# Kernel tuning notes

Measured on AMD Instinct MI355X. Metric: run time of the kernel, lower is better.

## Reference

```python
import jax, jax.numpy as jnp
import numpy as np

N_ENT = 50000
N_REL = 500
DIM = 128
B = 1024
N_EDGES = 800000
BN_EPS = 1e-5


def setup_inputs() -> dict:
    key = jax.random.key(0)
    ks = jax.random.split(key, 12)
    return {
        "E_emb": jax.random.normal(ks[0], (N_ENT, DIM), jnp.float32),
        "R_emb": jax.random.normal(ks[1], (N_REL, DIM), jnp.float32),
        "W1": jax.random.normal(ks[2], (DIM, DIM), jnp.float32) / np.sqrt(DIM),
        "b1": jax.random.normal(ks[3], (DIM,), jnp.float32) * 0.01,
        "W2": jax.random.normal(ks[4], (DIM, DIM), jnp.float32) / np.sqrt(DIM),
        "b2": jax.random.normal(ks[5], (DIM,), jnp.float32) * 0.01,
        "W": jax.random.normal(ks[6], (DIM, DIM), jnp.float32) / np.sqrt(DIM),
        "adj_vals": jax.random.uniform(ks[7], (N_EDGES,), jnp.float32) / 16.0,
        "bn0_gamma": jnp.ones((DIM,), jnp.float32),
        "bn0_beta": jnp.zeros((DIM,), jnp.float32),
        "bn1_gamma": jnp.ones((DIM,), jnp.float32),
        "bn1_beta": jnp.zeros((DIM,), jnp.float32),
        "batch_head": jax.random.randint(ks[8], (B,), 0, N_ENT, jnp.int32),
        "batch_rel": jax.random.randint(ks[9], (B,), 0, N_REL, jnp.int32),
        "init_ind": jnp.arange(N_ENT, dtype=jnp.int32),
        "adj_rows": jax.random.randint(ks[10], (N_EDGES,), 0, N_ENT, jnp.int32),
        "adj_cols": jax.random.randint(ks[11], (N_EDGES,), 0, N_ENT, jnp.int32),
    }


def _bn_eval(x, gamma, beta):
    # BatchNorm1d in eval mode with running_mean=0, running_var=1
    return x * (gamma / jnp.sqrt(1.0 + BN_EPS)) + beta


def _spmm(rows, cols, vals, dense):
    # out[i] = sum_{e: rows[e]==i} vals[e] * dense[cols[e]]
    gathered = dense[cols] * vals[:, None]  # [E, DIM]
    return jax.ops.segment_sum(gathered, rows, num_segments=N_ENT)


def reference(E_emb, R_emb, W1, b1, W2, b2, W, adj_vals,
              bn0_gamma, bn0_beta, bn1_gamma, bn1_beta,
              batch_head, batch_rel, init_ind, adj_rows, adj_cols):
    init_emb = E_emb[init_ind]                                  # [N, D]
    h = jax.nn.relu(_spmm(adj_rows, adj_cols, adj_vals, init_emb @ W1) + b1)
    h = jax.nn.relu(_spmm(adj_rows, adj_cols, adj_vals, h @ W2) + b2)
    final_emb = init_emb + h                                    # shortcut connection
    x = _bn_eval(final_emb[batch_head], bn0_gamma, bn0_beta)    # [B, D]
    r = R_emb[batch_rel]                                        # [B, D]
    W_mat = r @ W                                               # mat_vec_mul: [B, D]
    vm = _bn_eval(x * W_mat, bn1_gamma, bn1_beta)               # [B, D]
    dot = vm @ final_emb.T                                      # [B, N]
    return jax.nn.sigmoid(dot)
```

## Files before the change

kernel.cpp:

```cpp
#include <hip/hip_runtime.h>

#define N_ENT   50000
#define N_REL   500
#define N_EDGES 800000
#define DIM     128
#define BATCH   1024

typedef _Float16 half_t;
typedef __attribute__((ext_vector_type(8))) _Float16 half8;
typedef __attribute__((ext_vector_type(2))) _Float16 half2v;
typedef __attribute__((ext_vector_type(4))) float float4v;
typedef __attribute__((ext_vector_type(2))) float float2v;
typedef __attribute__((ext_vector_type(2))) int int2v;

__global__ __launch_bounds__(256) void k_pre(
        const int* __restrict__ rows, int* __restrict__ deg,
        const float* __restrict__ W1, const float* __restrict__ W2,
        half_t* __restrict__ W1T_hi, half_t* __restrict__ W1T_lo,
        half_t* __restrict__ W2T_hi, half_t* __restrict__ W2T_lo,
        const float* __restrict__ R_emb, const float* __restrict__ W,
        const int* __restrict__ rel, float* __restrict__ Wr){
    int blk = blockIdx.x;
    if(blk < 3125){
        int e = blk*256 + threadIdx.x;
        if(e < N_EDGES) atomicAdd(&deg[rows[e]], 1);
    } else if(blk < 3253){
        int i = (blk-3125)*256 + threadIdx.x;
        const float* src = (i < 16384) ? W1 : W2;
        half_t* dh = (i < 16384) ? W1T_hi : W2T_hi;
        half_t* dl = (i < 16384) ? W1T_lo : W2T_lo;
        int j = i & 16383;
        int d = j >> 7, c = j & 127;
        float f = src[j];
        half_t h = (half_t)f;
        dh[c*DIM + d] = h;
        dl[c*DIM + d] = (half_t)(f - (float)h);
    } else {
        __shared__ float rs[2][DIM];
        int half_id = threadIdx.x >> 7;
        int bb = (blk-3253)*2 + half_id;
        int j = threadIdx.x & 127;
        int rid = rel[bb];
        rs[half_id][j] = R_emb[rid*DIM + j];
        __syncthreads();
        float acc = 0.f;
        #pragma unroll 8
        for(int d=0; d<DIM; d++) acc += rs[half_id][d] * W[d*DIM + j];
        Wr[bb*DIM + j] = acc;
    }
}

__global__ __launch_bounds__(1024) void k_scan_mm1(
        const int* __restrict__ deg, int* __restrict__ row_start,
        const float* __restrict__ E, const int* __restrict__ init_ind,
        const half_t* __restrict__ WT_hi, const half_t* __restrict__ WT_lo,
        half_t* __restrict__ t_out){
    if(blockIdx.x == 0){
        __shared__ int part[1024];
        const int CH = 49;
        int t = threadIdx.x;
        int base = t*CH;
        int s = 0;
        for(int i=0;i<CH;i++){ int idx=base+i; if(idx<N_ENT) s += deg[idx]; }
        part[t]=s; __syncthreads();
        for(int off=1; off<1024; off<<=1){
            int v = part[t];
            int add = (t>=off)? part[t-off] : 0;
            __syncthreads();
            part[t] = v+add;
            __syncthreads();
        }
        int run = part[t]-s;
        for(int i=0;i<CH;i++){
            int idx=base+i;
            if(idx<=N_ENT){
                row_start[idx]=run;
                if(idx<N_ENT) run += deg[idx];
            }
        }
        return;
    }
    int wave = threadIdx.x >> 6, lane = threadIdx.x & 63;
    int mt = (blockIdx.x-1)*16 + wave;
    if(mt >= 3125) return;
    int m = lane & 15, q = lane >> 4;
    int row = init_ind[mt*16 + m];
    const float* ap = E + (long)row*DIM + q*8;
    float4v acc[8];
    #pragma unroll
    for(int i=0;i<8;i++) acc[i] = (float4v){0.f,0.f,0.f,0.f};
    #pragma unroll
    for(int ks=0; ks<4; ks++){
        float4v u0 = *(const float4v*)(ap + ks*32);
        float4v u1 = *(const float4v*)(ap + ks*32 + 4);
        half8 ah, al;
        #pragma unroll
        for(int j=0;j<8;j++){
            float fv = (j<4) ? u0[j] : u1[j-4];
            half_t h = (half_t)fv;
            ah[j] = h;
            al[j] = (half_t)(fv - (float)h);
        }
        #pragma unroll
        for(int nt=0; nt<8; nt++){
            half8 bh = *(const half8*)(WT_hi + (nt*16 + m)*DIM + ks*32 + q*8);
            half8 bl = *(const half8*)(WT_lo + (nt*16 + m)*DIM + ks*32 + q*8);
            acc[nt] = __builtin_amdgcn_mfma_f32_16x16x32_f16(ah, bh, acc[nt], 0,0,0);
            acc[nt] = __builtin_amdgcn_mfma_f32_16x16x32_f16(ah, bl, acc[nt], 0,0,0);
            acc[nt] = __builtin_amdgcn_mfma_f32_16x16x32_f16(al, bh, acc[nt], 0,0,0);
        }
    }
    #pragma unroll
    for(int nt=0; nt<8; nt++)
        #pragma unroll
        for(int r=0;r<4;r++)
            t_out[(mt*16 + q*4 + r)*DIM + nt*16 + m] = (half_t)acc[nt][r];
}

__global__ __launch_bounds__(256) void k_scatter(const int* __restrict__ rows,
        const int* __restrict__ cols, const float* __restrict__ vals,
        const int* __restrict__ row_start, int* __restrict__ cursor,
        int2v* __restrict__ csr){
    int e = blockIdx.x*256 + threadIdx.x;
    if(e >= N_EDGES) return;
    int r = rows[e];
    int pos = row_start[r] + atomicAdd(&cursor[r], 1);
    int2v p;
    p[0] = cols[e];
    p[1] = __float_as_int(vals[e]);
    csr[pos] = p;
}

__global__ __launch_bounds__(256) void k_sp1mm2(
        const half_t* __restrict__ t, const int* __restrict__ row_start,
        const int2v* __restrict__ csr, const float* __restrict__ b1,
        const half_t* __restrict__ WT_hi, const half_t* __restrict__ WT_lo,
        half_t* __restrict__ t2){
    __shared__ half_t hh[16][136];
    __shared__ half_t hl[16][136];
    int wave = threadIdx.x>>6, lane = threadIdx.x&63;
    int mt = blockIdx.x;
    const half2v* tp = (const half2v*)t;
    float2v bb = *(const float2v*)(b1 + lane*2);
    for(int rr=0; rr<4; rr++){
        int i = mt*16 + wave*4 + rr;
        int e0 = __builtin_amdgcn_readfirstlane(row_start[i]);
        int e1 = __builtin_amdgcn_readfirstlane(row_start[i+1]);
        float a0=0.f, a1=0.f;
        int e = e0;
        for(; e+8<=e1; e+=8){
            int2v p0=csr[e],   p1=csr[e+1], p2=csr[e+2], p3=csr[e+3];
            int2v p4=csr[e+4], p5=csr[e+5], p6=csr[e+6], p7=csr[e+7];
            half2v g0=tp[p0[0]*64+lane], g1=tp[p1[0]*64+lane], g2=tp[p2[0]*64+lane], g3=tp[p3[0]*64+lane];
            half2v g4=tp[p4[0]*64+lane], g5=tp[p5[0]*64+lane], g6=tp[p6[0]*64+lane], g7=tp[p7[0]*64+lane];
            float v0=__int_as_float(p0[1]), v1=__int_as_float(p1[1]), v2=__int_as_float(p2[1]), v3=__int_as_float(p3[1]);
            float v4=__int_as_float(p4[1]), v5=__int_as_float(p5[1]), v6=__int_as_float(p6[1]), v7=__int_as_float(p7[1]);
            a0 += v0*(float)g0[0]; a1 += v0*(float)g0[1];
            a0 += v1*(float)g1[0]; a1 += v1*(float)g1[1];
            a0 += v2*(float)g2[0]; a1 += v2*(float)g2[1];
            a0 += v3*(float)g3[0]; a1 += v3*(float)g3[1];
            a0 += v4*(float)g4[0]; a1 += v4*(float)g4[1];
            a0 += v5*(float)g5[0]; a1 += v5*(float)g5[1];
            a0 += v6*(float)g6[0]; a1 += v6*(float)g6[1];
            a0 += v7*(float)g7[0]; a1 += v7*(float)g7[1];
        }
        for(; e+4<=e1; e+=4){
            int2v p0=csr[e], p1=csr[e+1], p2=csr[e+2], p3=csr[e+3];
            half2v g0=tp[p0[0]*64+lane], g1=tp[p1[0]*64+lane], g2=tp[p2[0]*64+lane], g3=tp[p3[0]*64+lane];
            float v0=__int_as_float(p0[1]), v1=__int_as_float(p1[1]), v2=__int_as_float(p2[1]), v3=__int_as_float(p3[1]);
            a0 += v0*(float)g0[0]; a1 += v0*(float)g0[1];
            a0 += v1*(float)g1[0]; a1 += v1*(float)g1[1];
            a0 += v2*(float)g2[0]; a1 += v2*(float)g2[1];
            a0 += v3*(float)g3[0]; a1 += v3*(float)g3[1];
        }
        for(; e<e1; e++){
            int2v p = csr[e];
            half2v g = tp[p[0]*64+lane];
            float v = __int_as_float(p[1]);
            a0 += v*(float)g[0]; a1 += v*(float)g[1];
        }
        float r0 = fmaxf(a0 + bb[0], 0.f);
        float r1 = fmaxf(a1 + bb[1], 0.f);
        half_t h0=(half_t)r0, h1=(half_t)r1;
        int row = wave*4 + rr;
        *(half2v*)&hh[row][lane*2] = (half2v){h0, h1};
        *(half2v*)&hl[row][lane*2] = (half2v){(half_t)(r0-(float)h0), (half_t)(r1-(float)h1)};
    }
    __syncthreads();
    int m = lane & 15, q = lane >> 4;
    float4v acc[2];
    acc[0] = (float4v){0.f,0.f,0.f,0.f};
    acc[1] = (float4v){0.f,0.f,0.f,0.f};
    #pragma unroll
    for(int ks=0; ks<4; ks++){
        half8 ah = *(const half8*)&hh[m][ks*32 + q*8];
        half8 al = *(const half8*)&hl[m][ks*32 + q*8];
        #pragma unroll
        for(int n=0; n<2; n++){
            int nt = wave*2 + n;
            half8 bh = *(const half8*)(WT_hi + (nt*16 + m)*DIM + ks*32 + q*8);
            half8 bl = *(const half8*)(WT_lo + (nt*16 + m)*DIM + ks*32 + q*8);
            acc[n] = __builtin_amdgcn_mfma_f32_16x16x32_f16(ah, bh, acc[n], 0,0,0);
            acc[n] = __builtin_amdgcn_mfma_f32_16x16x32_f16(ah, bl, acc[n], 0,0,0);
            acc[n] = __builtin_amdgcn_mfma_f32_16x16x32_f16(al, bh, acc[n], 0,0,0);
        }
    }
    #pragma unroll
    for(int n=0; n<2; n++){
        int nt = wave*2 + n;
        #pragma unroll
        for(int r=0;r<4;r++)
            t2[(mt*16 + q*4 + r)*DIM + nt*16 + m] = (half_t)acc[n][r];
    }
}

__global__ __launch_bounds__(256) void k_spmm2(const half_t* __restrict__ t,
        const int* __restrict__ row_start, const int2v* __restrict__ csr,
        const float* __restrict__ b2_, const float* __restrict__ E,
        const int* __restrict__ init_ind,
        half_t* __restrict__ fe_hi, half_t* __restrict__ fe_lo){
    int wave = threadIdx.x>>6, lane = threadIdx.x&63;
    int i = blockIdx.x*4 + wave;
    if(i >= N_ENT) return;
    int e0 = __builtin_amdgcn_readfirstlane(row_start[i]);
    int e1 = __builtin_amdgcn_readfirstlane(row_start[i+1]);
    const half2v* tp = (const half2v*)t;
    float a0=0.f, a1=0.f;
    int e = e0;
    for(; e+8<=e1; e+=8){
        int2v p0=csr[e],   p1=csr[e+1], p2=csr[e+2], p3=csr[e+3];
        int2v p4=csr[e+4], p5=csr[e+5], p6=csr[e+6], p7=csr[e+7];
        half2v g0=tp[p0[0]*64+lane], g1=tp[p1[0]*64+lane], g2=tp[p2[0]*64+lane], g3=tp[p3[0]*64+lane];
        half2v g4=tp[p4[0]*64+lane], g5=tp[p5[0]*64+lane], g6=tp[p6[0]*64+lane], g7=tp[p7[0]*64+lane];
        float v0=__int_as_float(p0[1]), v1=__int_as_float(p1[1]), v2=__int_as_float(p2[1]), v3=__int_as_float(p3[1]);
        float v4=__int_as_float(p4[1]), v5=__int_as_float(p5[1]), v6=__int_as_float(p6[1]), v7=__int_as_float(p7[1]);
        a0 += v0*(float)g0[0]; a1 += v0*(float)g0[1];
        a0 += v1*(float)g1[0]; a1 += v1*(float)g1[1];
        a0 += v2*(float)g2[0]; a1 += v2*(float)g2[1];
        a0 += v3*(float)g3[0]; a1 += v3*(float)g3[1];
        a0 += v4*(float)g4[0]; a1 += v4*(float)g4[1];
        a0 += v5*(float)g5[0]; a1 += v5*(float)g5[1];
        a0 += v6*(float)g6[0]; a1 += v6*(float)g6[1];
        a0 += v7*(float)g7[0]; a1 += v7*(float)g7[1];
    }
    for(; e+4<=e1; e+=4){
        int2v p0=csr[e], p1=csr[e+1], p2=csr[e+2], p3=csr[e+3];
        half2v g0=tp[p0[0]*64+lane], g1=tp[p1[0]*64+lane], g2=tp[p2[0]*64+lane], g3=tp[p3[0]*64+lane];
        float v0=__int_as_float(p0[1]), v1=__int_as_float(p1[1]), v2=__int_as_float(p2[1]), v3=__int_as_float(p3[1]);
        a0 += v0*(float)g0[0]; a1 += v0*(float)g0[1];
        a0 += v1*(float)g1[0]; a1 += v1*(float)g1[1];
        a0 += v2*(float)g2[0]; a1 += v2*(float)g2[1];
        a0 += v3*(float)g3[0]; a1 += v3*(float)g3[1];
    }
    for(; e<e1; e++){
        int2v p = csr[e];
        half2v g = tp[p[0]*64+lane];
        float v = __int_as_float(p[1]);
        a0 += v*(float)g[0]; a1 += v*(float)g[1];
    }
    int erow = init_ind[i];
    float2v ev = *(const float2v*)(E + (long)erow*DIM + lane*2);
    float2v bb = *(const float2v*)(b2_ + lane*2);
    float f0 = ev[0] + fmaxf(a0 + bb[0], 0.f);
    float f1 = ev[1] + fmaxf(a1 + bb[1], 0.f);
    half_t h0=(half_t)f0, h1=(half_t)f1;
    half2v hi = {h0, h1};
    half2v lo = {(half_t)(f0-(float)h0), (half_t)(f1-(float)h1)};
    *(half2v*)(fe_hi + (long)i*DIM + lane*2) = hi;
    *(half2v*)(fe_lo + (long)i*DIM + lane*2) = lo;
}

__global__ __launch_bounds__(256) void k_vm(const float* __restrict__ Wr,
        const int* __restrict__ head, const half_t* __restrict__ fe_hi,
        const half_t* __restrict__ fe_lo, const float* __restrict__ g0v,
        const float* __restrict__ be0, const float* __restrict__ g1v,
        const float* __restrict__ be1, half_t* __restrict__ vm_hi,
        half_t* __restrict__ vm_lo){
    int idx = blockIdx.x*256 + threadIdx.x;
    int b = idx >> 7, j = idx & 127;
    int hid = head[b];
    const float inv = rsqrtf(1.f + 1e-5f);
    float fe = (float)fe_hi[(long)hid*DIM+j] + (float)fe_lo[(long)hid*DIM+j];
    float x  = fe * (g0v[j] * inv) + be0[j];
    float vmv = (x * Wr[idx]) * (g1v[j] * inv) + be1[j];
    half_t hi = (half_t)vmv;
    vm_hi[idx] = hi;
    vm_lo[idx] = (half_t)(vmv - (float)hi);
}

__global__ __launch_bounds__(256) void k_big(const half_t* __restrict__ vm_hi,
        const half_t* __restrict__ vm_lo, const half_t* __restrict__ fe_h,
        float* __restrict__ out){
    __shared__ float sl[16*260];
    int wave = threadIdx.x>>6, lane = threadIdx.x&63;
    int m = lane&15, q = lane>>4;
    int b0 = blockIdx.y * 64;
    int n0 = blockIdx.x * 256 + wave*64;
    float4v acc[4][4];
    #pragma unroll
    for(int a=0;a<4;a++)
        #pragma unroll
        for(int b=0;b<4;b++) acc[a][b] = (float4v){0.f,0.f,0.f,0.f};
    #pragma unroll
    for(int ks=0; ks<4; ks++){
        half8 B[4], Ah[4], Al[4];
        #pragma unroll
        for(int nt=0;nt<4;nt++){
            int nr = n0 + nt*16 + m;
            if(nr > N_ENT-1) nr = N_ENT-1;
            B[nt] = *(const half8*)(fe_h + (long)nr*DIM + ks*32 + q*8);
        }
        #pragma unroll
        for(int mt=0;mt<4;mt++){
            long ao = (long)(b0 + mt*16 + m)*DIM + ks*32 + q*8;
            Ah[mt] = *(const half8*)(vm_hi + ao);
            Al[mt] = *(const half8*)(vm_lo + ao);
        }
        #pragma unroll
        for(int mt=0;mt<4;mt++)
            #pragma unroll
            for(int nt=0;nt<4;nt++){
                acc[mt][nt] = __builtin_amdgcn_mfma_f32_16x16x32_f16(Ah[mt], B[nt], acc[mt][nt], 0,0,0);
                acc[mt][nt] = __builtin_amdgcn_mfma_f32_16x16x32_f16(Al[mt], B[nt], acc[mt][nt], 0,0,0);
            }
    }
    int gcol = blockIdx.x*256 + lane*4;
    #pragma unroll
    for(int mt=0; mt<4; mt++){
        if(mt) __syncthreads();
        #pragma unroll
        for(int nt=0;nt<4;nt++)
            #pragma unroll
            for(int r=0;r<4;r++){
                float d = acc[mt][nt][r];
                float s = __fdividef(1.f, 1.f + __expf(-d));
                sl[(q*4+r)*260 + wave*64 + nt*16 + m] = s;
            }
        __syncthreads();
        if(gcol < N_ENT){
            #pragma unroll
            for(int k=0;k<4;k++){
                int lr = wave*4 + k;
                float4v vv = *(const float4v*)&sl[lr*260 + lane*4];
                long off = (long)(b0 + mt*16 + lr)*N_ENT + gcol;
                __builtin_nontemporal_store(vv, (float4v*)(out + off));
            }
        }
    }
}

extern "C" void kernel_launch(void* const* d_in, const int* in_sizes, int n_in,
                              void* d_out, int out_size, void* d_ws, size_t ws_size,
                              hipStream_t stream) {
    const float* E     = (const float*)d_in[0];
    const float* R_emb = (const float*)d_in[1];
    const float* W1    = (const float*)d_in[2];
    const float* b1    = (const float*)d_in[3];
    const float* W2    = (const float*)d_in[4];
    const float* b2_   = (const float*)d_in[5];
    const float* W     = (const float*)d_in[6];
    const float* vals  = (const float*)d_in[7];
    const float* g0v   = (const float*)d_in[8];
    const float* be0   = (const float*)d_in[9];
    const float* g1v   = (const float*)d_in[10];
    const float* be1   = (const float*)d_in[11];
    const int* head    = (const int*)d_in[12];
    const int* rel     = (const int*)d_in[13];
    const int* init_ind= (const int*)d_in[14];
    const int* rows    = (const int*)d_in[15];
    const int* cols    = (const int*)d_in[16];
    float* out = (float*)d_out;

    char* w = (char*)d_ws;
    int*    deg       = (int*)   (w + 0);
    int*    cursor    = (int*)   (w + 200000);
    int*    row_start = (int*)   (w + 400000);
    int2v*  csr       = (int2v*) (w + 600064);
    half_t* W1T_hi    = (half_t*)(w + 7000064);
    half_t* W1T_lo    = (half_t*)(w + 7032832);
    half_t* W2T_hi    = (half_t*)(w + 7065600);
    half_t* W2T_lo    = (half_t*)(w + 7098368);
    float*  Wr        = (float*) (w + 7131136);
    half_t* t         = (half_t*)(w + 7655424);
    half_t* t2        = (half_t*)(w + 20455424);
    half_t* fe_hi     = (half_t*)(w + 33255424);
    half_t* fe_lo     = (half_t*)(w + 46055424);
    half_t* vm_hi     = (half_t*)(w + 58855424);
    half_t* vm_lo     = (half_t*)(w + 59117568);

    hipMemsetAsync(deg, 0, 2*N_ENT*sizeof(int), stream);
    k_pre      <<<3765, 256, 0, stream>>>(rows, deg, W1, W2, W1T_hi, W1T_lo, W2T_hi, W2T_lo,
                                          R_emb, W, rel, Wr);
    k_scan_mm1 <<<197, 1024, 0, stream>>>(deg, row_start, E, init_ind, W1T_hi, W1T_lo, t);
    k_scatter  <<<3125, 256, 0, stream>>>(rows, cols, vals, row_start, cursor, csr);
    k_sp1mm2   <<<3125, 256, 0, stream>>>(t, row_start, csr, b1, W2T_hi, W2T_lo, t2);
    k_spmm2    <<<12500, 256, 0, stream>>>(t2, row_start, csr, b2_, E, init_ind, fe_hi, fe_lo);
    k_vm       <<<512, 256, 0, stream>>>(Wr, head, fe_hi, fe_lo, g0v, be0, g1v, be1, vm_hi, vm_lo);
    k_big      <<<dim3(196, 16), 256, 0, stream>>>(vm_hi, vm_lo, fe_hi, out);
}
```

Before: 560.1 us.

## Use one wave per row in fused SpMM+GEMM and swizzle big-GEMM block order

The fused sparse-aggregate plus W2 GEMM kernel now launches 1024-thread blocks: 16 waves each gather one row instead of 4 waves gathering 4 rows sequentially. Eight of those waves then each compute one 16-column MFMA tile. This exposes more memory-level parallelism in the latency-bound gather, at the cost of idle waves during the MFMA phase and heavier per-block resource needs. The final scoring GEMM is launched as a flat 1D grid with a swizzle that spreads consecutive blocks across 8 groups, apparently to improve cache locality or XCD distribution of the shared operand tiles.

```diff
diff --git a/kernel.cpp b/kernel.cpp
--- a/kernel.cpp
+++ b/kernel.cpp
@@ -131,7 +131,7 @@
     csr[pos] = p;
 }
 
-__global__ __launch_bounds__(256) void k_sp1mm2(
+__global__ __launch_bounds__(1024) void k_sp1mm2(
         const half_t* __restrict__ t, const int* __restrict__ row_start,
         const int2v* __restrict__ csr, const float* __restrict__ b1,
         const half_t* __restrict__ WT_hi, const half_t* __restrict__ WT_lo,
@@ -142,8 +142,8 @@
     int mt = blockIdx.x;
     const half2v* tp = (const half2v*)t;
     float2v bb = *(const float2v*)(b1 + lane*2);
-    for(int rr=0; rr<4; rr++){
-        int i = mt*16 + wave*4 + rr;
+    {
+        int i = mt*16 + wave;
         int e0 = __builtin_amdgcn_readfirstlane(row_start[i]);
         int e1 = __builtin_amdgcn_readfirstlane(row_start[i+1]);
         float a0=0.f, a1=0.f;
@@ -182,35 +182,27 @@
         float r0 = fmaxf(a0 + bb[0], 0.f);
         float r1 = fmaxf(a1 + bb[1], 0.f);
         half_t h0=(half_t)r0, h1=(half_t)r1;
-        int row = wave*4 + rr;
-        *(half2v*)&hh[row][lane*2] = (half2v){h0, h1};
-        *(half2v*)&hl[row][lane*2] = (half2v){(half_t)(r0-(float)h0), (half_t)(r1-(float)h1)};
+        *(half2v*)&hh[wave][lane*2] = (half2v){h0, h1};
+        *(half2v*)&hl[wave][lane*2] = (half2v){(half_t)(r0-(float)h0), (half_t)(r1-(float)h1)};
     }
     __syncthreads();
-    int m = lane & 15, q = lane >> 4;
-    float4v acc[2];
-    acc[0] = (float4v){0.f,0.f,0.f,0.f};
-    acc[1] = (float4v){0.f,0.f,0.f,0.f};
-    #pragma unroll
-    for(int ks=0; ks<4; ks++){
-        half8 ah = *(const half8*)&hh[m][ks*32 + q*8];
-        half8 al = *(const half8*)&hl[m][ks*32 + q*8];
-        #pragma unroll
-        for(int n=0; n<2; n++){
-            int nt = wave*2 + n;
+    if(wave < 8){
+        int m = lane & 15, q = lane >> 4;
+        int nt = wave;
+        float4v acc = (float4v){0.f,0.f,0.f,0.f};
+        #pragma unroll
+        for(int ks=0; ks<4; ks++){
+            half8 ah = *(const half8*)&hh[m][ks*32 + q*8];
+            half8 al = *(const half8*)&hl[m][ks*32 + q*8];
             half8 bh = *(const half8*)(WT_hi + (nt*16 + m)*DIM + ks*32 + q*8);
             half8 bl = *(const half8*)(WT_lo + (nt*16 + m)*DIM + ks*32 + q*8);
-            acc[n] = __builtin_amdgcn_mfma_f32_16x16x32_f16(ah, bh, acc[n], 0,0,0);
-            acc[n] = __builtin_amdgcn_mfma_f32_16x16x32_f16(ah, bl, acc[n], 0,0,0);
-            acc[n] = __builtin_amdgcn_mfma_f32_16x16x32_f16(al, bh, acc[n], 0,0,0);
-        }
-    }
-    #pragma unroll
-    for(int n=0; n<2; n++){
-        int nt = wave*2 + n;
+            acc = __builtin_amdgcn_mfma_f32_16x16x32_f16(ah, bh, acc, 0,0,0);
+            acc = __builtin_amdgcn_mfma_f32_16x16x32_f16(ah, bl, acc, 0,0,0);
+            acc = __builtin_amdgcn_mfma_f32_16x16x32_f16(al, bh, acc, 0,0,0);
+        }
         #pragma unroll
         for(int r=0;r<4;r++)
-            t2[(mt*16 + q*4 + r)*DIM + nt*16 + m] = (half_t)acc[n][r];
+            t2[(mt*16 + q*4 + r)*DIM + nt*16 + m] = (half_t)acc[r];
     }
 }
 
@@ -292,10 +284,14 @@
         const half_t* __restrict__ vm_lo, const half_t* __restrict__ fe_h,
         float* __restrict__ out){
     __shared__ float sl[16*260];
+    int flat = blockIdx.x;
+    int wg = (flat & 7)*392 + (flat >> 3);
+    int bx = wg >> 4;
+    int by = wg & 15;
     int wave = threadIdx.x>>6, lane = threadIdx.x&63;
     int m = lane&15, q = lane>>4;
-    int b0 = blockIdx.y * 64;
-    int n0 = blockIdx.x * 256 + wave*64;
+    int b0 = by * 64;
+    int n0 = bx * 256 + wave*64;
     float4v acc[4][4];
     #pragma unroll
     for(int a=0;a<4;a++)
@@ -324,7 +320,7 @@
                 acc[mt][nt] = __builtin_amdgcn_mfma_f32_16x16x32_f16(Al[mt], B[nt], acc[mt][nt], 0,0,0);
             }
     }
-    int gcol = blockIdx.x*256 + lane*4;
+    int gcol = bx*256 + lane*4;
     #pragma unroll
     for(int mt=0; mt<4; mt++){
         if(mt) __syncthreads();
@@ -393,8 +389,8 @@
                                           R_emb, W, rel, Wr);
     k_scan_mm1 <<<197, 1024, 0, stream>>>(deg, row_start, E, init_ind, W1T_hi, W1T_lo, t);
     k_scatter  <<<3125, 256, 0, stream>>>(rows, cols, vals, row_start, cursor, csr);
-    k_sp1mm2   <<<3125, 256, 0, stream>>>(t, row_start, csr, b1, W2T_hi, W2T_lo, t2);
+    k_sp1mm2   <<<3125, 1024, 0, stream>>>(t, row_start, csr, b1, W2T_hi, W2T_lo, t2);
     k_spmm2    <<<12500, 256, 0, stream>>>(t2, row_start, csr, b2_, E, init_ind, fe_hi, fe_lo);
     k_vm       <<<512, 256, 0, stream>>>(Wr, head, fe_hi, fe_lo, g0v, be0, g1v, be1, vm_hi, vm_lo);
-    k_big      <<<dim3(196, 16), 256, 0, stream>>>(vm_hi, vm_lo, fe_hi, out);
-}
+    k_big      <<<3136, 256, 0, stream>>>(vm_hi, vm_lo, fe_hi, out);
+}
```

New measurement: 557.4 us. No clear change (-0.5%).
